# Performance work log

Measured on AMD Instinct MI355X. Metric: run time of the kernel, lower is better.

Reference implementation:

```python
import jax, jax.numpy as jnp
import numpy as np

B, N = 32, 1024
NUM = B * N
DIMS = [(1, 128, 8), (128, 128, 8), (128, 64, 16), (64, 64, 16), (64, 32, 1)]  # (cin, cout, heads)

def _edges():
    # bidirectional chain per batch element, offset by N per graph (as in torch forward)
    a = np.arange(N - 1)
    offs = (np.arange(B) * N)[:, None]
    src = np.concatenate([(a[None] + offs).ravel(), (a[None] + 1 + offs).ravel()])
    dst = np.concatenate([(a[None] + 1 + offs).ravel(), (a[None] + offs).ravel()])
    return jnp.asarray(src, jnp.int32), jnp.asarray(dst, jnp.int32)

def _conv(x, src, dst, Wm, bm, Ws, bs, att):
    # PyG GeneralConv: directed msg, additive attention, aggr='add', head-mean, + lin_self
    h, cout = att.shape
    m = (x @ Wm + bm)[src].reshape(-1, h, cout)          # [E, H, C] edge messages
    m = jnp.where(m > 0, m, 0.01 * m)                    # F.leaky_relu default slope 0.01
    alpha = jnp.einsum('ehc,hc->eh', m, att)             # [E, H] attention logits
    amax = jax.ops.segment_max(alpha, dst, num_segments=NUM)
    ex = jnp.exp(alpha - amax[dst])
    den = jax.ops.segment_sum(ex, dst, num_segments=NUM)
    w = ex / (den[dst] + 1e-16)                          # segment softmax over incoming edges
    agg = jax.ops.segment_sum(m * w[:, :, None], dst, num_segments=NUM)  # [NUM, H, C]
    return agg.mean(axis=1) + x @ Ws + bs                # head mean + self loop linear

def _forward(nodes, params, Wc, bc):
    src, dst = _edges()
    x = nodes.reshape(NUM, 1)
    for i, p in enumerate(params):
        x = _conv(x, src, dst, *p)
        if i < 4:
            x = jax.nn.elu(x)                            # Dropout(0.4) identity at eval
    out = x.reshape(B, N, -1)[:, -1, :]                  # last node per graph -> [B, 32]
    return out @ Wc + bc, out

def setup_inputs():
    key = jax.random.key(0)
    ks = jax.random.split(key, 20)
    inp = {"nodes": jax.random.normal(ks[0], (B, N), dtype=jnp.float32)}
    i = 1
    for l, (cin, cout, h) in enumerate(DIMS, 1):
        s = float(1.0 / np.sqrt(cin))
        inp["Wm%d" % l] = jax.random.uniform(ks[i], (cin, h * cout), jnp.float32, -s, s); i += 1
        inp["bm%d" % l] = jnp.zeros((h * cout,), jnp.float32)
        inp["Ws%d" % l] = jax.random.uniform(ks[i], (cin, cout), jnp.float32, -s, s); i += 1
        inp["bs%d" % l] = jnp.zeros((cout,), jnp.float32)
        inp["att%d" % l] = jax.random.normal(ks[i], (h, cout), jnp.float32) * 0.1; i += 1
    inp["Wc"] = jax.random.normal(ks[i], (32, 1), jnp.float32) * 0.1
    inp["bc"] = jnp.zeros((1,), jnp.float32)
    return inp

def reference(nodes, Wm1, bm1, Ws1, bs1, att1, Wm2, bm2, Ws2, bs2, att2, Wm3, bm3, Ws3, bs3, att3, Wm4, bm4, Ws4, bs4, att4, Wm5, bm5, Ws5, bs5, att5, Wc, bc):
    params = [(Wm1, bm1, Ws1, bs1, att1), (Wm2, bm2, Ws2, bs2, att2), (Wm3, bm3, Ws3, bs3, att3), (Wm4, bm4, Ws4, bs4, att4), (Wm5, bm5, Ws5, bs5, att5)]
    return _forward(nodes, params, Wc, bc)
```

## Files before the change

kernel.cpp:

```cpp
#include <hip/hip_runtime.h>

#define BATCH 32
#define NLEN  1024
#define NUMV  (BATCH * NLEN)

typedef __attribute__((ext_vector_type(8))) short short8;
typedef __attribute__((ext_vector_type(4))) float f32x4;

__device__ inline unsigned short rne_bf16(float x) {
    union { float f; unsigned u; } a; a.f = x;
    return (unsigned short)((a.u + 0x7FFFu + ((a.u >> 16) & 1u)) >> 16);
}
__device__ inline void bsplit(float x, unsigned short& h, unsigned short& l) {
    union { float f; unsigned u; } a; a.f = x;
    unsigned hb = (a.u + 0x7FFFu + ((a.u >> 16) & 1u)) & 0xFFFF0000u;
    h = (unsigned short)(hb >> 16);
    union { unsigned u; float f; } hf; hf.u = hb;
    l = rne_bf16(x - hf.f);
}
__device__ inline float bf16_to_f(unsigned short v) {
    union { unsigned u; float f; } a; a.u = ((unsigned)v) << 16; return a.f;
}

template<int CIN, int COUT, int H>
__device__ void pack_layer(const float* __restrict__ Wm, const float* __restrict__ Ws,
                           unsigned short* __restrict__ out, int t0, int nthr)
{
    constexpr int HC = H * COUT;
    constexpr int KC = ((CIN + 31) & ~31) / 32;
    constexpr int NT = (HC + COUT) / 16;
    const int total = NT * KC * 1024;
    for (int f = t0; f < total; f += nthr) {
        int j  = f & 7;
        int c  = (f >> 3) & 15;
        int g  = (f >> 7) & 3;
        int hl = (f >> 9) & 1;
        int r2 = f >> 10;
        int kc = r2 % KC, nt = r2 / KC;
        int k = kc * 32 + g * 8 + j, col = nt * 16 + c;
        float v = 0.f;
        if (k < CIN) v = (col < HC) ? Wm[k * HC + col] : Ws[k * COUT + (col - HC)];
        unsigned short h, l; bsplit(v, h, l);
        out[f] = hl ? l : h;
    }
}

__global__ void pack_all(const float* Wm1, const float* Ws1, const float* Wm2, const float* Ws2,
                         const float* Wm3, const float* Ws3, const float* Wm4, const float* Ws4,
                         unsigned short* p1, unsigned short* p2, unsigned short* p3, unsigned short* p4)
{
    int t = blockIdx.x * 256 + threadIdx.x;
    int n = gridDim.x * 256;
    pack_layer<1, 128, 8>(Wm1, Ws1, p1, t, n);
    pack_layer<128, 128, 8>(Wm2, Ws2, p2, t, n);
    pack_layer<128, 64, 16>(Wm3, Ws3, p3, t, n);
    pack_layer<64, 64, 16>(Wm4, Ws4, p4, t, n);
}

template<int CIN, int COUT, int H, bool MPACK>
__global__ __launch_bounds__(256, 3)
void conv_reg(const float* __restrict__ x, const unsigned short* __restrict__ pw,
              const float* __restrict__ bm, const float* __restrict__ bs,
              const float* __restrict__ att, float* __restrict__ y)
{
    constexpr int HC = H * COUT;
    static_assert(HC == 1024, "");
    constexpr int KC   = ((CIN + 31) & ~31) / 32;
    constexpr int HT   = COUT / 16;
    constexpr int MT   = HC / 16;
    constexpr int NTOT = MT + HT;
    constexpr int ROWSB = 56;
    constexpr int TPG  = (NLEN + ROWSB - 1) / ROWSB;
    constexpr int PL   = HC + COUT;
    constexpr float invH = 1.0f / H;

    const int tid  = threadIdx.x;
    const int lane = tid & 63;
    const int w    = tid >> 6;
    const int r    = lane & 15;
    const int gg   = lane >> 4;
    const int g    = blockIdx.x / TPG;
    const int n0   = (blockIdx.x % TPG) * ROWSB;
    const size_t gstart = (size_t)g * NLEN;

    __shared__ alignas(8) float pl[PL * 2];

    for (int i = tid; i < PL; i += 256) {
        float a, b;
        if (i < HC) { a = bm[i]; b = att[i]; }
        else        { a = bs[i - HC]; b = 0.f; }
        pl[2 * i] = a; pl[2 * i + 1] = b;
    }

    short8 a_hi[KC], a_lo[KC];
    {
        const int na = n0 - 1 + w * 14 + r;
        const bool av = (na >= 0) && (na < NLEN);
        const float* xrow = x + (gstart + (size_t)(av ? na : 0)) * CIN;
        #pragma unroll
        for (int kc = 0; kc < KC; kc++) {
            float vals[8];
            if constexpr (CIN % 32 == 0) {
                if (av) {
                    f32x4 v0 = *(const f32x4*)(xrow + kc * 32 + gg * 8);
                    f32x4 v1 = *(const f32x4*)(xrow + kc * 32 + gg * 8 + 4);
                    vals[0]=v0[0]; vals[1]=v0[1]; vals[2]=v0[2]; vals[3]=v0[3];
                    vals[4]=v1[0]; vals[5]=v1[1]; vals[6]=v1[2]; vals[7]=v1[3];
                } else {
                    #pragma unroll
                    for (int jj = 0; jj < 8; jj++) vals[jj] = 0.f;
                }
            } else {
                #pragma unroll
                for (int jj = 0; jj < 8; jj++) {
                    int k = kc * 32 + gg * 8 + jj;
                    vals[jj] = (av && k < CIN) ? xrow[k] : 0.f;
                }
            }
            union { short8 v; unsigned short u[8]; } hu, lu;
            #pragma unroll
            for (int jj = 0; jj < 8; jj++) bsplit(vals[jj], hu.u[jj], lu.u[jj]);
            a_hi[kc] = hu.v; a_lo[kc] = lu.v;
        }
    }

    float out[HT][4];
    #pragma unroll
    for (int q = 0; q < HT; q++)
        #pragma unroll
        for (int e = 0; e < 4; e++) out[q][e] = 0.f;

    float    mf[MPACK ? 1 : HT][4];
    unsigned mpk[MPACK ? HT : 1][2];

    __syncthreads();

    const int boff = gg * 128 + r * 8;

    short8 b0h[KC], b0l[KC], b1h[KC], b1l[KC];

    auto loadB = [&](short8 (&dh)[KC], short8 (&dl)[KC], int nt) {
        const unsigned short* tb = pw + (size_t)nt * (KC * 1024);
        #pragma unroll
        for (int kc = 0; kc < KC; kc++) {
            dh[kc] = *(const short8*)&tb[(kc * 2 + 0) * 512 + boff];
            dl[kc] = *(const short8*)&tb[(kc * 2 + 1) * 512 + boff];
        }
    };
    auto mfma3 = [&](short8 (&bh)[KC], short8 (&bl)[KC], float seed) -> f32x4 {
        f32x4 acc0 = {seed, seed, seed, seed};
        f32x4 acc1 = {0.f, 0.f, 0.f, 0.f};
        f32x4 acc2 = {0.f, 0.f, 0.f, 0.f};
        #pragma unroll
        for (int kc = 0; kc < KC; kc++) {
            acc0 = __builtin_amdgcn_mfma_f32_16x16x32_bf16(a_hi[kc], bh[kc], acc0, 0, 0, 0);
            acc1 = __builtin_amdgcn_mfma_f32_16x16x32_bf16(a_hi[kc], bl[kc], acc1, 0, 0, 0);
            acc2 = __builtin_amdgcn_mfma_f32_16x16x32_bf16(a_lo[kc], bh[kc], acc2, 0, 0, 0);
        }
        return acc0 + acc1 + acc2;
    };
    auto msgTile = [&](short8 (&bh)[KC], short8 (&bl)[KC], int nt, float (&p)[4]) -> f32x4 {
        const float2 pv = *(const float2*)&pl[(nt * 16 + r) * 2];
        f32x4 vv = mfma3(bh, bl, pv.x);
        #pragma unroll
        for (int e = 0; e < 4; e++) {
            float v = vv[e];
            v = v > 0.f ? v : 0.01f * v;
            vv[e] = v;
            p[e] += v * pv.y;
        }
        return vv;
    };
    auto storeM = [&](int q, f32x4 vv) {
        if constexpr (MPACK) {
            mpk[q][0] = ((unsigned)rne_bf16(vv[1]) << 16) | rne_bf16(vv[0]);
            mpk[q][1] = ((unsigned)rne_bf16(vv[3]) << 16) | rne_bf16(vv[2]);
        } else {
            #pragma unroll
            for (int e = 0; e < 4; e++) mf[q][e] = vv[e];
        }
    };

    loadB(b0h, b0l, 0);

    for (int h = 0; h < H; h++) {
        float p[4] = {0.f, 0.f, 0.f, 0.f};
        #pragma unroll
        for (int qq = 0; qq < HT; qq += 2) {
            const int nt0 = h * HT + qq;
            loadB(b1h, b1l, nt0 + 1);
            storeM(qq, msgTile(b0h, b0l, nt0, p));
            if (nt0 + 2 < NTOT) loadB(b0h, b0l, nt0 + 2);
            storeM(qq + 1, msgTile(b1h, b1l, nt0 + 1, p));
        }
        #pragma unroll
        for (int e = 0; e < 4; e++) {
            float v = p[e];
            v += __shfl_xor(v, 1, 64);
            v += __shfl_xor(v, 2, 64);
            v += __shfl_xor(v, 4, 64);
            v += __shfl_xor(v, 8, 64);
            p[e] = v;
        }
        {
            const int jbase = w * 14;
            float a3u = __shfl_up(p[3], 16, 64);
            float a0d = __shfl_down(p[0], 16, 64);
            float wpv[4], wnv[4];
            #pragma unroll
            for (int e = 0; e < 4; e++) {
                const int jr = gg * 4 + e;
                const int nl = n0 - 1 + jbase + jr;
                const bool hp = nl >= 1;
                const bool hn = nl < NLEN - 1;
                float ap = (e > 0) ? p[e - 1] : a3u;
                float an = (e < 3) ? p[e + 1] : a0d;
                float apx = hp ? ap : -1e30f;
                float anx = hn ? an : -1e30f;
                float mx = fmaxf(apx, anx);
                float ep = hp ? __expf(ap - mx) : 0.f;
                float en = hn ? __expf(an - mx) : 0.f;
                float inv = 1.f / (ep + en + 1e-16f);
                wpv[e] = ep * inv; wnv[e] = en * inv;
            }
            #pragma unroll
            for (int q = 0; q < HT; q++) {
                float v0, v1, v2, v3;
                if constexpr (MPACK) {
                    v0 = bf16_to_f((unsigned short)(mpk[q][0] & 0xffff));
                    v1 = bf16_to_f((unsigned short)(mpk[q][0] >> 16));
                    v2 = bf16_to_f((unsigned short)(mpk[q][1] & 0xffff));
                    v3 = bf16_to_f((unsigned short)(mpk[q][1] >> 16));
                } else {
                    v0 = mf[q][0]; v1 = mf[q][1]; v2 = mf[q][2]; v3 = mf[q][3];
                }
                float m3u = __shfl_up(v3, 16, 64);
                float m0d = __shfl_down(v0, 16, 64);
                float mvals[4] = {v0, v1, v2, v3};
                #pragma unroll
                for (int e = 0; e < 4; e++) {
                    float mprev = (e > 0) ? mvals[e - 1] : m3u;
                    float mnext = (e < 3) ? mvals[e + 1] : m0d;
                    out[q][e] += wpv[e] * mprev + wnv[e] * mnext;
                }
            }
        }
    }

    auto selfTile = [&](short8 (&bh)[KC], short8 (&bl)[KC], int q2) {
        const int c2 = q2 * 16 + r;
        const float bsv = pl[(HC + c2) * 2];
        f32x4 acc = mfma3(bh, bl, bsv);
        const int jbase = w * 14;
        #pragma unroll
        for (int e = 0; e < 4; e++) {
            const int jr = gg * 4 + e;
            const int nl = n0 - 1 + jbase + jr;
            float v = out[q2][e] * invH + acc[e];
            v = v > 0.f ? v : __expf(v) - 1.f;
            if (jr >= 1 && jr <= 14 && nl < NLEN)
                y[(gstart + nl) * COUT + c2] = v;
        }
    };
    #pragma unroll
    for (int q2 = 0; q2 < HT; q2 += 2) {
        const int nt0 = MT + q2;
        loadB(b1h, b1l, nt0 + 1);
        selfTile(b0h, b0l, q2);
        if (nt0 + 2 < NTOT) loadB(b0h, b0l, nt0 + 2);
        selfTile(b1h, b1l, q2 + 1);
    }
}

__global__ void final_head(const float* __restrict__ x4,
                           const float* __restrict__ Wm,
                           const float* __restrict__ bm,
                           const float* __restrict__ Ws,
                           const float* __restrict__ bs,
                           const float* __restrict__ Wc,
                           const float* __restrict__ bc,
                           float* __restrict__ out)
{
    int g = blockIdx.x;
    int c = threadIdx.x;
    const float* xu = &x4[((long)g * NLEN + NLEN - 2) * 64];
    const float* xv = xu + 64;
    float o = 0.f;
    if (c < 32) {
        float m = bm[c];
        float s = bs[c];
        for (int k = 0; k < 64; k++) {
            m = fmaf(xu[k], Wm[k * 32 + c], m);
            s = fmaf(xv[k], Ws[k * 32 + c], s);
        }
        m = m > 0.f ? m : 0.01f * m;
        o = m + s;
        out[32 + g * 32 + c] = o;
    }
    float tsum = (c < 32) ? o * Wc[c] : 0.f;
    #pragma unroll
    for (int sft = 16; sft > 0; sft >>= 1)
        tsum += __shfl_xor(tsum, sft, 64);
    if (c == 0) out[g] = tsum + bc[0];
}

extern "C" void kernel_launch(void* const* d_in, const int* in_sizes, int n_in,
                              void* d_out, int out_size, void* d_ws, size_t ws_size,
                              hipStream_t stream)
{
    const float* nodes = (const float*)d_in[0];
    auto L = [&](int l, int k) { return (const float*)d_in[1 + (l - 1) * 5 + k]; };

    float* xb0 = (float*)d_ws;
    float* xb1 = xb0 + (size_t)NUMV * 128;
    unsigned short* p1 = (unsigned short*)(xb1 + (size_t)NUMV * 128);
    unsigned short* p2 = p1 + 72 * 1024;
    unsigned short* p3 = p2 + 72 * 4096;
    unsigned short* p4 = p3 + 68 * 4096;

    pack_all<<<dim3(512), dim3(256), 0, stream>>>(
        L(1,0), L(1,2), L(2,0), L(2,2), L(3,0), L(3,2), L(4,0), L(4,2), p1, p2, p3, p4);

    constexpr int TPG = (NLEN + 55) / 56;
    dim3 grid(BATCH * TPG);
    dim3 blk(256);

    conv_reg<1,   128, 8,  false><<<grid, blk, 0, stream>>>(nodes, p1, L(1,1), L(1,3), L(1,4), xb0);
    conv_reg<128, 128, 8,  true ><<<grid, blk, 0, stream>>>(xb0,   p2, L(2,1), L(2,3), L(2,4), xb1);
    conv_reg<128, 64,  16, false><<<grid, blk, 0, stream>>>(xb1,   p3, L(3,1), L(3,3), L(3,4), xb0);
    conv_reg<64,  64,  16, false><<<grid, blk, 0, stream>>>(xb0,   p4, L(4,1), L(4,3), L(4,4), xb1);

    final_head<<<dim3(BATCH), dim3(64), 0, stream>>>(
        xb1, L(5,0), L(5,1), L(5,2), L(5,3),
        (const float*)d_in[26], (const float*)d_in[27], (float*)d_out);
}
```

Measured before the change: 397.6 us.

## Stage packed weight tiles through LDS double buffer and drop lo*lo-free third accumulator

Weight tiles were previously loaded by every wave straight from global memory into registers. They are now loaded cooperatively by the whole block into registers, written to a double-buffered LDS array with explicit vmcnt waits and barriers, and read from LDS by each wave. The intent is to cut redundant global and L2 traffic across the four waves. The two correction MFMAs now share one accumulator, and occupancy is lowered to 2 blocks per SIMD via launch bounds to make room for the staging. This adds a block barrier per tile and LDS capacity pressure, and the hand-written waitcnt logic is fragile.

```diff
diff --git a/kernel.cpp b/kernel.cpp
--- a/kernel.cpp
+++ b/kernel.cpp
@@ -20,6 +20,13 @@
 }
 __device__ inline float bf16_to_f(unsigned short v) {
     union { unsigned u; float f; } a; a.u = ((unsigned)v) << 16; return a.f;
+}
+
+template<int N> __device__ __forceinline__ void wait_vmcnt() {
+    if constexpr (N == 0)      asm volatile("s_waitcnt vmcnt(0)" ::: "memory");
+    else if constexpr (N == 1) asm volatile("s_waitcnt vmcnt(1)" ::: "memory");
+    else if constexpr (N == 2) asm volatile("s_waitcnt vmcnt(2)" ::: "memory");
+    else static_assert(N <= 2, "");
 }
 
 template<int CIN, int COUT, int H>
@@ -58,7 +65,7 @@
 }
 
 template<int CIN, int COUT, int H, bool MPACK>
-__global__ __launch_bounds__(256, 3)
+__global__ __launch_bounds__(256, 2)
 void conv_reg(const float* __restrict__ x, const unsigned short* __restrict__ pw,
               const float* __restrict__ bm, const float* __restrict__ bs,
               const float* __restrict__ att, float* __restrict__ y)
@@ -69,6 +76,8 @@
     constexpr int HT   = COUT / 16;
     constexpr int MT   = HC / 16;
     constexpr int NTOT = MT + HT;
+    constexpr int NCH  = KC * 128;
+    constexpr int CHPT = (NCH + 255) / 256;
     constexpr int ROWSB = 56;
     constexpr int TPG  = (NLEN + ROWSB - 1) / ROWSB;
     constexpr int PL   = HC + COUT;
@@ -83,6 +92,7 @@
     const int n0   = (blockIdx.x % TPG) * ROWSB;
     const size_t gstart = (size_t)g * NLEN;
 
+    __shared__ alignas(16) unsigned short bufs[2][KC * 1024];
     __shared__ alignas(8) float pl[PL * 2];
 
     for (int i = tid; i < PL; i += 256) {
@@ -133,35 +143,45 @@
     float    mf[MPACK ? 1 : HT][4];
     unsigned mpk[MPACK ? HT : 1][2];
 
-    __syncthreads();
-
     const int boff = gg * 128 + r * 8;
 
-    short8 b0h[KC], b0l[KC], b1h[KC], b1l[KC];
-
-    auto loadB = [&](short8 (&dh)[KC], short8 (&dl)[KC], int nt) {
-        const unsigned short* tb = pw + (size_t)nt * (KC * 1024);
+    f32x4 sA[CHPT], sB[CHPT];
+
+    auto issueLoads = [&](f32x4 (&s)[CHPT], int nt) {
+        const f32x4* ps = (const f32x4*)pw + (size_t)nt * NCH;
+        #pragma unroll
+        for (int i = 0; i < CHPT; i++) { int idx = tid + i * 256; if (idx < NCH) s[i] = ps[idx]; }
+    };
+    auto writeLds = [&](f32x4 (&s)[CHPT], int par) {
+        #pragma unroll
+        for (int i = 0; i < CHPT; i++) { int idx = tid + i * 256; if (idx < NCH) *(f32x4*)&bufs[par][idx * 8] = s[i]; }
+    };
+    auto fence = [&]() {
+        asm volatile("s_waitcnt lgkmcnt(0)" ::: "memory");
+        __builtin_amdgcn_sched_barrier(0);
+        __builtin_amdgcn_s_barrier();
+        __builtin_amdgcn_sched_barrier(0);
+    };
+    auto mfma2 = [&](int par, float seed) -> f32x4 {
+        short8 bh[KC], bl[KC];
         #pragma unroll
         for (int kc = 0; kc < KC; kc++) {
-            dh[kc] = *(const short8*)&tb[(kc * 2 + 0) * 512 + boff];
-            dl[kc] = *(const short8*)&tb[(kc * 2 + 1) * 512 + boff];
-        }
-    };
-    auto mfma3 = [&](short8 (&bh)[KC], short8 (&bl)[KC], float seed) -> f32x4 {
+            bh[kc] = *(const short8*)&bufs[par][(kc * 2 + 0) * 512 + boff];
+            bl[kc] = *(const short8*)&bufs[par][(kc * 2 + 1) * 512 + boff];
+        }
         f32x4 acc0 = {seed, seed, seed, seed};
         f32x4 acc1 = {0.f, 0.f, 0.f, 0.f};
-        f32x4 acc2 = {0.f, 0.f, 0.f, 0.f};
         #pragma unroll
         for (int kc = 0; kc < KC; kc++) {
             acc0 = __builtin_amdgcn_mfma_f32_16x16x32_bf16(a_hi[kc], bh[kc], acc0, 0, 0, 0);
             acc1 = __builtin_amdgcn_mfma_f32_16x16x32_bf16(a_hi[kc], bl[kc], acc1, 0, 0, 0);
-            acc2 = __builtin_amdgcn_mfma_f32_16x16x32_bf16(a_lo[kc], bh[kc], acc2, 0, 0, 0);
-        }
-        return acc0 + acc1 + acc2;
-    };
-    auto msgTile = [&](short8 (&bh)[KC], short8 (&bl)[KC], int nt, float (&p)[4]) -> f32x4 {
+            acc1 = __builtin_amdgcn_mfma_f32_16x16x32_bf16(a_lo[kc], bh[kc], acc1, 0, 0, 0);
+        }
+        return acc0 + acc1;
+    };
+    auto msgTile = [&](int q, int nt, int par, float (&p)[4]) {
         const float2 pv = *(const float2*)&pl[(nt * 16 + r) * 2];
-        f32x4 vv = mfma3(bh, bl, pv.x);
+        f32x4 vv = mfma2(par, pv.x);
         #pragma unroll
         for (int e = 0; e < 4; e++) {
             float v = vv[e];
@@ -169,9 +189,6 @@
             vv[e] = v;
             p[e] += v * pv.y;
         }
-        return vv;
-    };
-    auto storeM = [&](int q, f32x4 vv) {
         if constexpr (MPACK) {
             mpk[q][0] = ((unsigned)rne_bf16(vv[1]) << 16) | rne_bf16(vv[0]);
             mpk[q][1] = ((unsigned)rne_bf16(vv[3]) << 16) | rne_bf16(vv[2]);
@@ -180,18 +197,42 @@
             for (int e = 0; e < 4; e++) mf[q][e] = vv[e];
         }
     };
-
-    loadB(b0h, b0l, 0);
+    auto selfTile = [&](int q2, int par) {
+        const int c2 = q2 * 16 + r;
+        f32x4 acc = mfma2(par, pl[(HC + c2) * 2]);
+        const int jbase = w * 14;
+        #pragma unroll
+        for (int e = 0; e < 4; e++) {
+            const int jr = gg * 4 + e;
+            const int nl = n0 - 1 + jbase + jr;
+            float v = out[q2][e] * invH + acc[e];
+            v = v > 0.f ? v : __expf(v) - 1.f;
+            if (jr >= 1 && jr <= 14 && nl < NLEN)
+                y[(gstart + nl) * COUT + c2] = v;
+        }
+    };
+
+    issueLoads(sA, 0);
+    wait_vmcnt<0>();
+    writeLds(sA, 0);
+    issueLoads(sA, 1);
+    fence();
 
     for (int h = 0; h < H; h++) {
         float p[4] = {0.f, 0.f, 0.f, 0.f};
         #pragma unroll
         for (int qq = 0; qq < HT; qq += 2) {
-            const int nt0 = h * HT + qq;
-            loadB(b1h, b1l, nt0 + 1);
-            storeM(qq, msgTile(b0h, b0l, nt0, p));
-            if (nt0 + 2 < NTOT) loadB(b0h, b0l, nt0 + 2);
-            storeM(qq + 1, msgTile(b1h, b1l, nt0 + 1, p));
+            const int nt = h * HT + qq;
+            issueLoads(sB, nt + 2);
+            msgTile(qq, nt, 0, p);
+            wait_vmcnt<CHPT>();
+            writeLds(sA, 1);
+            fence();
+            issueLoads(sA, nt + 3);
+            msgTile(qq + 1, nt + 1, 1, p);
+            wait_vmcnt<CHPT>();
+            writeLds(sB, 0);
+            fence();
         }
         #pragma unroll
         for (int e = 0; e < 4; e++) {
@@ -247,28 +288,24 @@
         }
     }
 
-    auto selfTile = [&](short8 (&bh)[KC], short8 (&bl)[KC], int q2) {
-        const int c2 = q2 * 16 + r;
-        const float bsv = pl[(HC + c2) * 2];
-        f32x4 acc = mfma3(bh, bl, bsv);
-        const int jbase = w * 14;
-        #pragma unroll
-        for (int e = 0; e < 4; e++) {
-            const int jr = gg * 4 + e;
-            const int nl = n0 - 1 + jbase + jr;
-            float v = out[q2][e] * invH + acc[e];
-            v = v > 0.f ? v : __expf(v) - 1.f;
-            if (jr >= 1 && jr <= 14 && nl < NLEN)
-                y[(gstart + nl) * COUT + c2] = v;
-        }
-    };
     #pragma unroll
     for (int q2 = 0; q2 < HT; q2 += 2) {
-        const int nt0 = MT + q2;
-        loadB(b1h, b1l, nt0 + 1);
-        selfTile(b0h, b0l, q2);
-        if (nt0 + 2 < NTOT) loadB(b0h, b0l, nt0 + 2);
-        selfTile(b1h, b1l, q2 + 1);
+        const int nt = MT + q2;
+        constexpr int dummy = 0; (void)dummy;
+        const bool i1 = (nt + 2 < NTOT);
+        const bool i2 = (nt + 3 < NTOT);
+        if (i1) issueLoads(sB, nt + 2);
+        selfTile(q2, 0);
+        if (i1) wait_vmcnt<CHPT>(); else wait_vmcnt<0>();
+        writeLds(sA, 1);
+        fence();
+        if (i2) issueLoads(sA, nt + 3);
+        selfTile(q2 + 1, 1);
+        if (q2 + 2 < HT) {
+            if (i2) wait_vmcnt<CHPT>(); else wait_vmcnt<0>();
+            writeLds(sB, 0);
+            fence();
+        }
     }
 }
 
```

Result: no change. 404.6 us (+1.8%).
